# Optimization experiments

Hardware: AMD Instinct MI355X
Metric: run time of the kernel (lower is better)

## Reference

```python
import jax, jax.numpy as jnp
import numpy as np
import math

N_HEAD = 4
NORM_GROUPS = 32
EPS = 1e-5


def setup_inputs() -> dict:
    key = jax.random.key(0)
    ks = jax.random.split(key, 6)
    C = 256
    x = jax.random.normal(ks[0], (2, C, 64, 64), dtype=jnp.float32)
    gn_w = jnp.ones((C,), dtype=jnp.float32)
    gn_b = jnp.zeros((C,), dtype=jnp.float32)
    s = 1.0 / math.sqrt(C)
    wq = jax.random.normal(ks[1], (C, C), dtype=jnp.float32) * s
    wk = jax.random.normal(ks[2], (C, C), dtype=jnp.float32) * s
    wv = jax.random.normal(ks[3], (C, C), dtype=jnp.float32) * s
    wo = jax.random.normal(ks[4], (C, C), dtype=jnp.float32) * s
    bo = jnp.zeros((C,), dtype=jnp.float32)
    return {"x": x, "gn_w": gn_w, "gn_b": gn_b, "wq": wq, "wk": wk,
            "wv": wv, "wo": wo, "bo": bo}


def group_norm(x, w, b):
    bsz, c, h, wd = x.shape
    xg = x.reshape(bsz, NORM_GROUPS, c // NORM_GROUPS, h, wd)
    mu = jnp.mean(xg, axis=(2, 3, 4), keepdims=True)
    var = jnp.mean(jnp.square(xg - mu), axis=(2, 3, 4), keepdims=True)
    xn = ((xg - mu) * jax.lax.rsqrt(var + EPS)).reshape(bsz, c, h, wd)
    return xn * w[None, :, None, None] + b[None, :, None, None]


def conv1x1(x, w):
    # w: (out_ch, in_ch) applied pointwise
    return jnp.einsum('bchw,oc->bohw', x, w)


def reference(x, gn_w, gn_b, wq, wk, wv, wo, bo):
    bsz, c, h, w = x.shape
    hd = c // N_HEAD
    norm = group_norm(x, gn_w, gn_b)
    q = conv1x1(norm, wq).reshape(bsz, N_HEAD, hd, h, w)
    k = conv1x1(norm, wk).reshape(bsz, N_HEAD, hd, h, w)
    v = conv1x1(norm, wv).reshape(bsz, N_HEAD, hd, h, w)
    # scores over full spatial positions; NOTE: scaled by sqrt(channel), as in source
    scores = jnp.einsum('bnchw,bncxy->bnhwxy', q, k) / jnp.sqrt(jnp.float32(c))
    probs = jax.nn.softmax(scores.reshape(bsz, N_HEAD, h, w, h * w), axis=-1)
    probs = probs.reshape(bsz, N_HEAD, h, w, h, w)
    out = jnp.einsum('bnhwxy,bncxy->bnchw', probs, v).reshape(bsz, c, h, w)
    out = conv1x1(out, wo) + bo[None, :, None, None]
    return out + x
```

## Files before the change

### kernel.cpp

```cpp
#include <hip/hip_runtime.h>

typedef float f32x4 __attribute__((ext_vector_type(4)));
typedef float f32x16 __attribute__((ext_vector_type(16)));
typedef short bf16x8 __attribute__((ext_vector_type(8)));
typedef unsigned short u16;
typedef unsigned int u32;

#define MFMA(a, b, c) __builtin_amdgcn_mfma_f32_16x16x32_bf16((a), (b), (c), 0, 0, 0)
#define MFMA32(a, b, c) __builtin_amdgcn_mfma_f32_32x32x16_bf16((a), (b), (c), 0, 0, 0)

static __device__ __forceinline__ u16 f2bf(float f) {
    union { float f; u32 u; } v; v.f = f;
    u32 r = v.u + 0x7FFFu + ((v.u >> 16) & 1u);
    return (u16)(r >> 16);
}

static __device__ __forceinline__ u32 pkbf(float a, float b) {
    u32 ua = __float_as_uint(a) + 0x8000u;
    u32 ub = __float_as_uint(b) + 0x8000u;
    return __builtin_amdgcn_perm(ub, ua, 0x07060302);
}

__global__ __launch_bounds__(256) void wcvt_kernel(
    const float* __restrict__ wq, const float* __restrict__ wk,
    const float* __restrict__ wv, const float* __restrict__ wo,
    u16* __restrict__ Wbf) {
    int base = (blockIdx.x * 256 + threadIdx.x) * 4;
    int p = base >> 16;
    int off = base & 65535;
    const float* W = (p == 0) ? wq : ((p == 1) ? wk : ((p == 2) ? wv : wo));
    float sc = (p == 0) ? 0.0625f : 1.0f;
    float4 v = *(const float4*)(W + off);
    uint2 pk;
    pk.x = pkbf(v.x * sc, v.y * sc);
    pk.y = pkbf(v.z * sc, v.w * sc);
    *(uint2*)(Wbf + base) = pk;
}

__global__ __launch_bounds__(256) void gn_stats(
    const float* __restrict__ x, float2* __restrict__ part) {
    int blk = blockIdx.x;
    int bg = blk >> 2, quarter = blk & 3;
    const float* xp = x + (size_t)bg * 32768 + quarter * 8192;
    int t = threadIdx.x;

    float s = 0.f, ss = 0.f;
#pragma unroll
    for (int rep = 0; rep < 8; ++rep) {
        float4 v = *(const float4*)(xp + t * 4 + rep * 1024);
        s += v.x + v.y + v.z + v.w;
        ss += v.x * v.x + v.y * v.y + v.z * v.z + v.w * v.w;
    }
    for (int off = 1; off < 64; off <<= 1) {
        s += __shfl_xor(s, off);
        ss += __shfl_xor(ss, off);
    }
    __shared__ float red[8];
    int lane = t & 63, w = t >> 6;
    if (lane == 0) { red[w] = s; red[4 + w] = ss; }
    __syncthreads();
    if (t == 0) {
        part[blk] = make_float2(red[0] + red[1] + red[2] + red[3],
                                red[4] + red[5] + red[6] + red[7]);
    }
}

__global__ __launch_bounds__(256) void gn_apply(
    const float* __restrict__ x, const float* __restrict__ gw,
    const float* __restrict__ gb, const float2* __restrict__ part,
    u16* __restrict__ normT) {
    int s0 = blockIdx.x * 32;
    int b = blockIdx.y;
    int t = threadIdx.x;
    __shared__ u16 tile[32 * 264];
    __shared__ float2 gstat[32];

    if (t < 32) {
        float s = 0.f, ss = 0.f;
#pragma unroll
        for (int q = 0; q < 4; ++q) {
            float2 p = part[(b * 32 + t) * 4 + q];
            s += p.x; ss += p.y;
        }
        float mu = s * (1.f / 32768.f);
        float var = ss * (1.f / 32768.f) - mu * mu;
        gstat[t] = make_float2(mu, rsqrtf(var + 1e-5f));
    }
    __syncthreads();

    int sj = (t & 7) * 4;
#pragma unroll
    for (int i = 0; i < 8; ++i) {
        int c = (t >> 3) + 32 * i;
        float2 st = gstat[c >> 3];
        float wgt = gw[c] * st.y;
        float bia = gb[c] - st.x * wgt;
        float4 v = *(const float4*)(x + (size_t)(b * 256 + c) * 4096 + s0 + sj);
        tile[(sj + 0) * 264 + c] = f2bf(v.x * wgt + bia);
        tile[(sj + 1) * 264 + c] = f2bf(v.y * wgt + bia);
        tile[(sj + 2) * 264 + c] = f2bf(v.z * wgt + bia);
        tile[(sj + 3) * 264 + c] = f2bf(v.w * wgt + bia);
    }
    __syncthreads();
#pragma unroll
    for (int k = 0; k < 4; ++k) {
        int idx = t + 256 * k;
        int row = idx >> 5, ch = idx & 31;
        *(uint4*)(normT + ((size_t)(b * 4096 + s0 + row)) * 256 + ch * 8) =
            *(const uint4*)(tile + row * 264 + ch * 8);
    }
}

__global__ __launch_bounds__(256) void qkv_gemm(
    const u16* __restrict__ normT, const u16* __restrict__ Wbf,
    u16* __restrict__ Q, u16* __restrict__ K, u16* __restrict__ V) {
    int b = blockIdx.y & 1;
    int p = blockIdx.y >> 1;
    const u16* W = Wbf + p * 65536;
    int m0 = (blockIdx.x & 1) * 128;
    int n0 = (blockIdx.x >> 1) * 64;

    __shared__ u16 a_s[128 * 40];
    __shared__ u16 b_s[64 * 40];

    int t = threadIdx.x;
    int lane = t & 63, wave = t >> 6;
    int wm = wave & 1, wn = wave >> 1;
    int r = lane & 15, qd = lane >> 4;

    const u16* Bsrc = normT + (size_t)b * 4096 * 256;

    f32x4 acc[4][2];
#pragma unroll
    for (int i = 0; i < 4; ++i)
#pragma unroll
        for (int j = 0; j < 2; ++j) acc[i][j] = (f32x4){0.f, 0.f, 0.f, 0.f};

    int srow = t >> 1;
    int scp = (t & 1) * 16;

    for (int kk = 0; kk < 256; kk += 32) {
        __syncthreads();
        {
            const u16* src = W + (m0 + srow) * 256 + kk + scp;
            *(uint4*)(a_s + srow * 40 + scp) = *(const uint4*)(src);
            *(uint4*)(a_s + srow * 40 + scp + 8) = *(const uint4*)(src + 8);
        }
        if (t < 128) {
            const u16* src = Bsrc + (size_t)(n0 + srow) * 256 + kk + scp;
            *(uint4*)(b_s + srow * 40 + scp) = *(const uint4*)(src);
            *(uint4*)(b_s + srow * 40 + scp + 8) = *(const uint4*)(src + 8);
        }
        __syncthreads();

        bf16x8 af[4], bf[2];
#pragma unroll
        for (int mt = 0; mt < 4; ++mt)
            af[mt] = *(const bf16x8*)(a_s + (wm * 64 + mt * 16 + r) * 40 + qd * 8);
#pragma unroll
        for (int nt = 0; nt < 2; ++nt)
            bf[nt] = *(const bf16x8*)(b_s + (wn * 32 + nt * 16 + r) * 40 + qd * 8);
        if (p == 2) {
#pragma unroll
            for (int mt = 0; mt < 4; ++mt)
#pragma unroll
                for (int nt = 0; nt < 2; ++nt)
                    acc[mt][nt] = MFMA(bf[nt], af[mt], acc[mt][nt]);
        } else {
#pragma unroll
            for (int mt = 0; mt < 4; ++mt)
#pragma unroll
                for (int nt = 0; nt < 2; ++nt)
                    acc[mt][nt] = MFMA(af[mt], bf[nt], acc[mt][nt]);
        }
    }

    if (p < 2) {
        u16* dst = (p == 0) ? Q : K;
#pragma unroll
        for (int mt = 0; mt < 4; ++mt) {
#pragma unroll
            for (int nt = 0; nt < 2; ++nt) {
                int o0 = m0 + wm * 64 + mt * 16 + qd * 4;
                int s = n0 + wn * 32 + nt * 16 + r;
                int h = o0 >> 6, d0 = o0 & 63;
                uint2 pk;
                pk.x = pkbf(acc[mt][nt][0], acc[mt][nt][1]);
                pk.y = pkbf(acc[mt][nt][2], acc[mt][nt][3]);
                *(uint2*)(dst + ((size_t)((b * 4 + h) * 4096 + s)) * 64 + d0) = pk;
            }
        }
    } else {
#pragma unroll
        for (int mt = 0; mt < 4; ++mt) {
#pragma unroll
            for (int nt = 0; nt < 2; ++nt) {
                int o = m0 + wm * 64 + mt * 16 + r;
                int h = o >> 6, d = o & 63;
                int sb = n0 + wn * 32 + nt * 16 + qd * 4;
                uint2 pk;
                pk.x = pkbf(acc[mt][nt][0], acc[mt][nt][1]);
                pk.y = pkbf(acc[mt][nt][2], acc[mt][nt][3]);
                *(uint2*)(V + ((size_t)((b * 4 + h) * 64 + d)) * 4096 + sb) = pk;
            }
        }
    }
}

template <int QT>
__global__ __launch_bounds__(256, 2) void attn_kernel(
    const u16* __restrict__ Q, const u16* __restrict__ K,
    const u16* __restrict__ V, u16* __restrict__ Opart,
    float* __restrict__ Lpart, int nk32) {
    int bh = blockIdx.x & 7, sp = blockIdx.x >> 3;
    int qb = blockIdx.y;
    int t = threadIdx.x, lane = t & 63, w = t >> 6;
    int qn = lane & 31, h = lane >> 5;

    const size_t bhoff = (size_t)bh * 4096 * 64;
    int q0 = (qb * 4 + w) * (32 * QT);
    int kbase = sp * nk32 * 32;

    bf16x8 qf[QT][4];
#pragma unroll
    for (int qt = 0; qt < QT; ++qt)
#pragma unroll
        for (int c = 0; c < 4; ++c)
            qf[qt][c] = *(const bf16x8*)(Q + bhoff +
                (size_t)(q0 + qt * 32 + qn) * 64 + c * 16 + h * 8);

    f32x16 oacc[2][QT];
#pragma unroll
    for (int dt = 0; dt < 2; ++dt)
#pragma unroll
        for (int qt = 0; qt < QT; ++qt)
#pragma unroll
            for (int i = 0; i < 16; ++i) oacc[dt][qt][i] = 0.f;
    float lacc[QT];
#pragma unroll
    for (int qt = 0; qt < QT; ++qt) lacc[qt] = 0.f;

    const u16* Kp = K + bhoff;
    const u16* Vp = V + bhoff;

    for (int kt = 0; kt < nk32; ++kt) {
        int k0 = kbase + kt * 32;
        bf16x8 kf[4];
#pragma unroll
        for (int c = 0; c < 4; ++c)
            kf[c] = *(const bf16x8*)(Kp + (size_t)(k0 + qn) * 64 + c * 16 + h * 8);
        bf16x8 vf[2][2];
#pragma unroll
        for (int dt = 0; dt < 2; ++dt)
#pragma unroll
            for (int kc = 0; kc < 2; ++kc)
                vf[dt][kc] = *(const bf16x8*)(Vp +
                    (size_t)(dt * 32 + qn) * 4096 + k0 + kc * 16 + h * 8);

#pragma unroll
        for (int qt = 0; qt < QT; ++qt) {
            f32x16 s;
#pragma unroll
            for (int i = 0; i < 16; ++i) s[i] = 0.f;
#pragma unroll
            for (int c = 0; c < 4; ++c) s = MFMA32(kf[c], qf[qt][c], s);

            float e[16];
            float ls = 0.f;
#pragma unroll
            for (int i = 0; i < 16; ++i) { e[i] = __expf(s[i]); ls += e[i]; }
            lacc[qt] += ls;

            u32 p[8], rm[8];
#pragma unroll
            for (int i = 0; i < 8; ++i) p[i] = pkbf(e[2 * i], e[2 * i + 1]);
#pragma unroll
            for (int i = 0; i < 8; ++i)
                rm[i] = (u32)__shfl_xor((int)p[i], 32);

            u32 a0 = h ? rm[2] : p[0], a1 = h ? rm[3] : p[1];
            u32 a2 = h ? p[2] : rm[0], a3 = h ? p[3] : rm[1];
            u32 b0 = h ? rm[6] : p[4], b1 = h ? rm[7] : p[5];
            u32 b2 = h ? p[6] : rm[4], b3 = h ? p[7] : rm[5];
            uint4 pau = {a0, a1, a2, a3};
            uint4 pbu = {b0, b1, b2, b3};
            bf16x8 pA = *(const bf16x8*)&pau;
            bf16x8 pB = *(const bf16x8*)&pbu;

#pragma unroll
            for (int dt = 0; dt < 2; ++dt) {
                oacc[dt][qt] = MFMA32(vf[dt][0], pA, oacc[dt][qt]);
                oacc[dt][qt] = MFMA32(vf[dt][1], pB, oacc[dt][qt]);
            }
        }
    }

    float lfull[QT];
#pragma unroll
    for (int qt = 0; qt < QT; ++qt)
        lfull[qt] = lacc[qt] + __shfl_xor(lacc[qt], 32);

    __shared__ u16 osw[4][64 * 72];
    u16* my = osw[w];
#pragma unroll
    for (int qt = 0; qt < QT; ++qt) {
        int row = qt * 32 + qn;
#pragma unroll
        for (int dt = 0; dt < 2; ++dt) {
#pragma unroll
            for (int g = 0; g < 4; ++g) {
                int d0 = g * 8 + h * 4 + dt * 32;
                uint2 pk;
                pk.x = pkbf(oacc[dt][qt][4 * g], oacc[dt][qt][4 * g + 1]);
                pk.y = pkbf(oacc[dt][qt][4 * g + 2], oacc[dt][qt][4 * g + 3]);
                *(uint2*)(my + row * 72 + d0) = pk;
            }
        }
    }
    __syncthreads();

    size_t obase = ((size_t)sp * 8 + bh) * 4096 + q0;
#pragma unroll
    for (int rr = 0; rr < 4 * QT; ++rr) {
        int row = rr * 8 + (lane >> 3), ch = lane & 7;
        uint4 v = *(const uint4*)(my + row * 72 + ch * 8);
        *(uint4*)(Opart + (obase + row) * 64 + ch * 8) = v;
    }
    if (h == 0) {
#pragma unroll
        for (int qt = 0; qt < QT; ++qt)
            Lpart[obase + qt * 32 + qn] = lfull[qt];
    }
}

__global__ __launch_bounds__(256) void attn_combine(
    const u16* __restrict__ Opart, const float* __restrict__ Lpart,
    u16* __restrict__ attnT, int nsplit) {
    int t = threadIdx.x;
    int gr = blockIdx.x * 64 + (t >> 2);
    int d0 = (t & 3) * 16;

    float l = 0.f;
    for (int s = 0; s < nsplit; ++s) l += Lpart[(size_t)s * 32768 + gr];
    float inv = 1.f / l;

    float acc[16];
#pragma unroll
    for (int i = 0; i < 16; ++i) acc[i] = 0.f;
    for (int s = 0; s < nsplit; ++s) {
        const u16* p = Opart + ((size_t)s * 32768 + gr) * 64 + d0;
        uint4 a = *(const uint4*)(p);
        uint4 bq = *(const uint4*)(p + 8);
        const u32* ap = (const u32*)&a;
        const u32* bp = (const u32*)&bq;
#pragma unroll
        for (int j = 0; j < 4; ++j) {
            acc[2 * j]     += __uint_as_float(ap[j] << 16);
            acc[2 * j + 1] += __uint_as_float(ap[j] & 0xFFFF0000u);
            acc[8 + 2 * j]     += __uint_as_float(bp[j] << 16);
            acc[8 + 2 * j + 1] += __uint_as_float(bp[j] & 0xFFFF0000u);
        }
    }
    u32 pk[8];
#pragma unroll
    for (int j = 0; j < 8; ++j)
        pk[j] = pkbf(acc[2 * j] * inv, acc[2 * j + 1] * inv);

    int bh = gr >> 12, q = gr & 4095;
    int b = bh >> 2, hh = bh & 3;
    u16* dst = attnT + ((size_t)(b * 4096 + q)) * 256 + hh * 64 + d0;
    *(uint4*)(dst) = make_uint4(pk[0], pk[1], pk[2], pk[3]);
    *(uint4*)(dst + 8) = make_uint4(pk[4], pk[5], pk[6], pk[7]);
}

__global__ __launch_bounds__(256) void out_gemm(
    const u16* __restrict__ attnT, const u16* __restrict__ W3,
    const float* __restrict__ bo, const float* __restrict__ x,
    float* __restrict__ out) {
    int b = blockIdx.y;
    int m0 = (blockIdx.x & 3) * 64;
    int n0 = (blockIdx.x >> 2) * 64;

    __shared__ u16 a_s[64 * 40];
    __shared__ u16 b_s[64 * 40];

    int t = threadIdx.x;
    int lane = t & 63, wave = t >> 6;
    int wm = wave & 1, wn = wave >> 1;
    int r = lane & 15, qd = lane >> 4;

    const u16* Bsrc = attnT + (size_t)b * 4096 * 256;

    f32x4 acc[2][2];
#pragma unroll
    for (int i = 0; i < 2; ++i)
#pragma unroll
        for (int j = 0; j < 2; ++j) acc[i][j] = (f32x4){0.f, 0.f, 0.f, 0.f};

    int u = t & 127;
    int srow = u >> 1;
    int scp = (u & 1) * 16;

    for (int kk = 0; kk < 256; kk += 32) {
        __syncthreads();
        if (t < 128) {
            const u16* src = W3 + (m0 + srow) * 256 + kk + scp;
            *(uint4*)(a_s + srow * 40 + scp) = *(const uint4*)(src);
            *(uint4*)(a_s + srow * 40 + scp + 8) = *(const uint4*)(src + 8);
        } else {
            const u16* src = Bsrc + (size_t)(n0 + srow) * 256 + kk + scp;
            *(uint4*)(b_s + srow * 40 + scp) = *(const uint4*)(src);
            *(uint4*)(b_s + srow * 40 + scp + 8) = *(const uint4*)(src + 8);
        }
        __syncthreads();

        bf16x8 af[2], bf[2];
#pragma unroll
        for (int mt = 0; mt < 2; ++mt)
            af[mt] = *(const bf16x8*)(a_s + (wm * 32 + mt * 16 + r) * 40 + qd * 8);
#pragma unroll
        for (int nt = 0; nt < 2; ++nt)
            bf[nt] = *(const bf16x8*)(b_s + (wn * 32 + nt * 16 + r) * 40 + qd * 8);
#pragma unroll
        for (int mt = 0; mt < 2; ++mt)
#pragma unroll
            for (int nt = 0; nt < 2; ++nt)
                acc[mt][nt] = MFMA(af[mt], bf[nt], acc[mt][nt]);
    }

#pragma unroll
    for (int mt = 0; mt < 2; ++mt) {
#pragma unroll
        for (int nt = 0; nt < 2; ++nt) {
#pragma unroll
            for (int j = 0; j < 4; ++j) {
                int o = m0 + wm * 32 + mt * 16 + qd * 4 + j;
                int s = n0 + wn * 32 + nt * 16 + r;
                size_t idx = (size_t)(b * 256 + o) * 4096 + s;
                out[idx] = acc[mt][nt][j] + bo[o] + x[idx];
            }
        }
    }
}

extern "C" void kernel_launch(void* const* d_in, const int* in_sizes, int n_in,
                              void* d_out, int out_size, void* d_ws, size_t ws_size,
                              hipStream_t stream) {
    const float* x = (const float*)d_in[0];
    const float* gn_w = (const float*)d_in[1];
    const float* gn_b = (const float*)d_in[2];
    const float* wq = (const float*)d_in[3];
    const float* wk = (const float*)d_in[4];
    const float* wv = (const float*)d_in[5];
    const float* wo = (const float*)d_in[6];
    const float* bo = (const float*)d_in[7];
    float* out = (float*)d_out;

    char* ws = (char*)d_ws;
    u16* normT = (u16*)(ws);
    u16* attnT = (u16*)(ws);
    u16* Q     = (u16*)(ws + (4u << 20));
    u16* Kp    = (u16*)(ws + (8u << 20));
    u16* Vp    = (u16*)(ws + (12u << 20));
    u16* Wbf   = (u16*)(ws + (16u << 20));
    float2* part = (float2*)(ws + (16u << 20) + 524288);

    size_t opart_off = (size_t)17 << 20;
    size_t opart_bytes4 = 4ull * 8 * 4096 * 64 * 2;
    int nsplit = (ws_size >= opart_off + opart_bytes4 + 4ull * 32768 * 4 + 4096)
                     ? 4 : 2;
    u16* Opart = (u16*)(ws + opart_off);
    float* Lpart = (float*)(ws + opart_off + (size_t)nsplit * 8 * 4096 * 64 * 2);

    wcvt_kernel<<<256, 256, 0, stream>>>(wq, wk, wv, wo, Wbf);
    gn_stats<<<256, 256, 0, stream>>>(x, part);
    gn_apply<<<dim3(128, 2), 256, 0, stream>>>(x, gn_w, gn_b, part, normT);
    qkv_gemm<<<dim3(128, 6), 256, 0, stream>>>(normT, Wbf, Q, Kp, Vp);
    if (nsplit == 4) {
        attn_kernel<2><<<dim3(32, 16), 256, 0, stream>>>(Q, Kp, Vp, Opart, Lpart, 32);
    } else {
        attn_kernel<1><<<dim3(16, 32), 256, 0, stream>>>(Q, Kp, Vp, Opart, Lpart, 64);
    }
    attn_combine<<<512, 256, 0, stream>>>(Opart, Lpart, attnT, nsplit);
    out_gemm<<<dim3(256, 2), 256, 0, stream>>>(attnT, Wbf + 3 * 65536, bo, x, out);
}
```

Baseline: 172.7 us.

## Use exp2 with log2e-folded Q scale, permute V loads to drop shuffles, add 8-way split

Folds log2(e) into the Q weight scale so the softmax can use the native exp2 instruction instead of __expf. Reorders the V fragment loads so the P operand layout from the score MFMA matches directly, which removes the cross-lane shuffles and selects per tile. Adds an 8-way key split for attention when workspace allows, giving more blocks at the cost of more partial outputs for the combine step. The V loads become narrower 8-byte loads, and the combine kernel now has to read eight partials.

```diff
diff --git a/kernel.cpp b/kernel.cpp
--- a/kernel.cpp
+++ b/kernel.cpp
@@ -19,6 +19,11 @@
     u32 ua = __float_as_uint(a) + 0x8000u;
     u32 ub = __float_as_uint(b) + 0x8000u;
     return __builtin_amdgcn_perm(ub, ua, 0x07060302);
+}
+
+static __device__ __forceinline__ bf16x8 mk8(uint2 a, uint2 b) {
+    uint4 t = {a.x, a.y, b.x, b.y};
+    return *(const bf16x8*)&t;
 }
 
 __global__ __launch_bounds__(256) void wcvt_kernel(
@@ -29,7 +34,7 @@
     int p = base >> 16;
     int off = base & 65535;
     const float* W = (p == 0) ? wq : ((p == 1) ? wk : ((p == 2) ? wv : wo));
-    float sc = (p == 0) ? 0.0625f : 1.0f;
+    float sc = (p == 0) ? 0.09014009048f : 1.0f;
     float4 v = *(const float4*)(W + off);
     uint2 pk;
     pk.x = pkbf(v.x * sc, v.y * sc);
@@ -251,11 +256,11 @@
             kf[c] = *(const bf16x8*)(Kp + (size_t)(k0 + qn) * 64 + c * 16 + h * 8);
         bf16x8 vf[2][2];
 #pragma unroll
-        for (int dt = 0; dt < 2; ++dt)
-#pragma unroll
-            for (int kc = 0; kc < 2; ++kc)
-                vf[dt][kc] = *(const bf16x8*)(Vp +
-                    (size_t)(dt * 32 + qn) * 4096 + k0 + kc * 16 + h * 8);
+        for (int dt = 0; dt < 2; ++dt) {
+            const u16* vr = Vp + (size_t)(dt * 32 + qn) * 4096 + k0 + 4 * h;
+            vf[dt][0] = mk8(*(const uint2*)(vr), *(const uint2*)(vr + 8));
+            vf[dt][1] = mk8(*(const uint2*)(vr + 16), *(const uint2*)(vr + 24));
+        }
 
 #pragma unroll
         for (int qt = 0; qt < QT; ++qt) {
@@ -268,24 +273,19 @@
             float e[16];
             float ls = 0.f;
 #pragma unroll
-            for (int i = 0; i < 16; ++i) { e[i] = __expf(s[i]); ls += e[i]; }
+            for (int i = 0; i < 16; ++i) {
+                e[i] = __builtin_amdgcn_exp2f(s[i]);
+                ls += e[i];
+            }
             lacc[qt] += ls;
 
-            u32 p[8], rm[8];
+            u32 p[8];
 #pragma unroll
             for (int i = 0; i < 8; ++i) p[i] = pkbf(e[2 * i], e[2 * i + 1]);
-#pragma unroll
-            for (int i = 0; i < 8; ++i)
-                rm[i] = (u32)__shfl_xor((int)p[i], 32);
-
-            u32 a0 = h ? rm[2] : p[0], a1 = h ? rm[3] : p[1];
-            u32 a2 = h ? p[2] : rm[0], a3 = h ? p[3] : rm[1];
-            u32 b0 = h ? rm[6] : p[4], b1 = h ? rm[7] : p[5];
-            u32 b2 = h ? p[6] : rm[4], b3 = h ? p[7] : rm[5];
-            uint4 pau = {a0, a1, a2, a3};
-            uint4 pbu = {b0, b1, b2, b3};
-            bf16x8 pA = *(const bf16x8*)&pau;
-            bf16x8 pB = *(const bf16x8*)&pbu;
+            uint4 pa = {p[0], p[1], p[2], p[3]};
+            uint4 pb = {p[4], p[5], p[6], p[7]};
+            bf16x8 pA = *(const bf16x8*)&pa;
+            bf16x8 pB = *(const bf16x8*)&pb;
 
 #pragma unroll
             for (int dt = 0; dt < 2; ++dt) {
@@ -466,9 +466,12 @@
     float2* part = (float2*)(ws + (16u << 20) + 524288);
 
     size_t opart_off = (size_t)17 << 20;
-    size_t opart_bytes4 = 4ull * 8 * 4096 * 64 * 2;
-    int nsplit = (ws_size >= opart_off + opart_bytes4 + 4ull * 32768 * 4 + 4096)
-                     ? 4 : 2;
+    size_t ob8 = 8ull * 8 * 4096 * 64 * 2;
+    size_t ob4 = 4ull * 8 * 4096 * 64 * 2;
+    int nsplit;
+    if (ws_size >= opart_off + ob8 + 8ull * 32768 * 4 + 4096) nsplit = 8;
+    else if (ws_size >= opart_off + ob4 + 4ull * 32768 * 4 + 4096) nsplit = 4;
+    else nsplit = 2;
     u16* Opart = (u16*)(ws + opart_off);
     float* Lpart = (float*)(ws + opart_off + (size_t)nsplit * 8 * 4096 * 64 * 2);
 
@@ -476,7 +479,9 @@
     gn_stats<<<256, 256, 0, stream>>>(x, part);
     gn_apply<<<dim3(128, 2), 256, 0, stream>>>(x, gn_w, gn_b, part, normT);
     qkv_gemm<<<dim3(128, 6), 256, 0, stream>>>(normT, Wbf, Q, Kp, Vp);
-    if (nsplit == 4) {
+    if (nsplit == 8) {
+        attn_kernel<2><<<dim3(64, 16), 256, 0, stream>>>(Q, Kp, Vp, Opart, Lpart, 16);
+    } else if (nsplit == 4) {
         attn_kernel<2><<<dim3(32, 16), 256, 0, stream>>>(Q, Kp, Vp, Opart, Lpart, 32);
     } else {
         attn_kernel<1><<<dim3(16, 32), 256, 0, stream>>>(Q, Kp, Vp, Opart, Lpart, 64);
```

Result: slower. 203.7 us (+18.0%).
